# Kernel optimization log

Hardware: AMD Instinct MI355X
Metric: run time of the kernel (lower is better)

The kernel has to match this reference:

```python
import jax, jax.numpy as jnp
import numpy as np

SIGMA = 0.05  # gaussian bandwidth from the source


def _sqdist(a, b):
    # a: [B,N,D], b: [B,M,D] -> [B,N,M] squared euclidean distance
    a2 = jnp.sum(a * a, axis=-1)[:, :, None]
    b2 = jnp.sum(b * b, axis=-1)[:, None, :]
    return a2 + b2 - 2.0 * jnp.einsum('bnd,bmd->bnm', a, b)


def setup_inputs() -> dict:
    key = jax.random.key(0)
    k1, k2, k3, k4 = jax.random.split(key, 4)
    B, N, D = 2, 4096, 32
    points = jax.random.normal(k1, (B, N, 3), dtype=jnp.float32)
    pointfea1 = jax.random.normal(k2, (B, N, D), dtype=jnp.float32)
    pointfea2 = jax.random.normal(k3, (B, N, D), dtype=jnp.float32)
    weights = jax.random.uniform(k4, (B, N), dtype=jnp.float32) / N  # point-cloud mass weights
    return {"points": points, "pointfea1": pointfea1, "pointfea2": pointfea2, "weights": weights}


def reference(points, pointfea1, pointfea2, weights):
    # naive_corres: per-point spatial log-gaussian softmax vs feature log-softmax,
    # weighted squared difference, reduced over both pair axes -> [B]
    x = points / SIGMA
    point_loggauss = jax.nn.log_softmax(-_sqdist(x, x), axis=2)          # [B,N,N]
    fea_logsoftmax = jax.nn.log_softmax(-_sqdist(pointfea1, pointfea2), axis=2)  # [B,N,N]
    diff2 = (jnp.exp(point_loggauss) - jnp.exp(fea_logsoftmax)) ** 2
    l2_loss = jnp.sum(diff2 * weights[:, :, None], axis=2)  # sum over j
    return jnp.sum(l2_loss, axis=1)                          # sum over i -> [B]
```

## Files before the change

kernel.cpp:

```cpp
#include <hip/hip_runtime.h>

#define D    32
#define BLK  256
#define NCH  8
#define SJ   128

#define LOG2E 1.44269504088896340736f

typedef short  short8  __attribute__((ext_vector_type(8)));
typedef float  floatx4 __attribute__((ext_vector_type(4)));

__device__ __forceinline__ short f2bf(float v) {
    union { float f; unsigned u; } x; x.f = v;
    unsigned r = x.u + 0x7fffu + ((x.u >> 16) & 1u);
    return (short)(r >> 16);
}
__device__ __forceinline__ float bf2f(short h) {
    union { float f; unsigned u; } x;
    x.u = ((unsigned)(unsigned short)h) << 16;
    return x.f;
}
__device__ __forceinline__ float fast_exp2(float x) {
#if __has_builtin(__builtin_amdgcn_exp2f)
    return __builtin_amdgcn_exp2f(x);
#else
    return exp2f(x);
#endif
}

__global__ __launch_bounds__(BLK) void precompute_kernel(
    const float* __restrict__ points,
    const float* __restrict__ fea1,
    const float* __restrict__ fea2,
    float4* __restrict__ xp,
    float* __restrict__ f1n,
    float* __restrict__ f2n,
    float* __restrict__ acc,
    float* __restrict__ out,
    int BN, int Bsz)
{
    int r = blockIdx.x * BLK + threadIdx.x;
    if (r < Bsz) out[r] = 0.0f;
    if (r >= BN) return;
#pragma unroll
    for (int s = 0; s < 5; ++s) acc[s * BN + r] = 0.0f;

    const float s20 = 20.0f;
    float x = points[3*r+0] * s20;
    float y = points[3*r+1] * s20;
    float z = points[3*r+2] * s20;
    float4 v; v.x = x; v.y = y; v.z = z;
    v.w = (x*x + y*y + z*z) * LOG2E;
    xp[r] = v;

    const float4* p1 = (const float4*)(fea1 + (size_t)r * D);
    const float4* p2 = (const float4*)(fea2 + (size_t)r * D);
    float n1 = 0.f, n2 = 0.f;
#pragma unroll
    for (int k = 0; k < D/4; ++k) {
        float4 a = p1[k];
        float4 b = p2[k];
        n1 = fmaf(a.x,a.x, fmaf(a.y,a.y, fmaf(a.z,a.z, fmaf(a.w,a.w, n1))));
        n2 = fmaf(b.x,b.x, fmaf(b.y,b.y, fmaf(b.z,b.z, fmaf(b.w,b.w, n2))));
    }
    f1n[r] = n1 * LOG2E;
    f2n[r] = n2 * LOG2E;
}

__global__ __launch_bounds__(BLK) void pair_kernel(
    const float* __restrict__ fea1,
    const float* __restrict__ fea2,
    const float4* __restrict__ xp,
    const float* __restrict__ f1n,
    const float* __restrict__ f2n,
    float* __restrict__ acc,
    int N, int BN)
{
    __shared__ short  sHi[SJ * D];
    __shared__ short  sLo[SJ * D];
    __shared__ float4 sXJ[SJ];
    __shared__ float  sFN[SJ];

    const int tid  = threadIdx.x;
    const int lane = tid & 63;
    const int wv   = tid >> 6;
    const int m    = lane & 15;
    const int q    = lane >> 4;

    const int ibpb  = N / 64;
    const int b     = blockIdx.x / ibpb;
    const int ibase = blockIdx.x * 64 + wv * 16;
    const int JCH   = N / NCH;
    const int jc0   = blockIdx.y * JCH;

    const float* f1p = fea1 + (size_t)(ibase + m) * D + q * 8;
    float4 bv0 = *(const float4*)(f1p);
    float4 bv1 = *(const float4*)(f1p + 4);
    float bf[8] = {bv0.x,bv0.y,bv0.z,bv0.w,bv1.x,bv1.y,bv1.z,bv1.w};
    short8 Bhi, Blo;
#pragma unroll
    for (int k = 0; k < 8; ++k) {
        short h = f2bf(bf[k]);
        Bhi[k] = h;
        Blo[k] = f2bf(bf[k] - bf2f(h));
    }

    const float L2 = 2.0f * LOG2E;
    float4 xi = xp[ibase + m];
    float xix = xi.x * L2, xiy = xi.y * L2, xiz = xi.z * L2, xiw = xi.w;
    float nfi = -f1n[ibase + m];

    float sA = 0.f, s2a = 0.f, sB = 0.f, s2b = 0.f, sab = 0.f;

    const float*  f2b  = fea2 + (size_t)(b * N + jc0) * D;
    const float4* xpb  = xp  + (size_t)b * N + jc0;
    const float*  f2nb = f2n + (size_t)b * N + jc0;

    const int rowl = tid >> 3;
    const int c4   = (tid & 7) * 4;

    for (int s = 0; s < JCH; s += SJ) {
#pragma unroll
        for (int g = 0; g < SJ/32; ++g) {
            int r_ = g * 32 + rowl;
            float4 v = *(const float4*)(f2b + (size_t)(s + r_) * D + c4);
            short4 h, l;
            h.x = f2bf(v.x); l.x = f2bf(v.x - bf2f(h.x));
            h.y = f2bf(v.y); l.y = f2bf(v.y - bf2f(h.y));
            h.z = f2bf(v.z); l.z = f2bf(v.z - bf2f(h.z));
            h.w = f2bf(v.w); l.w = f2bf(v.w - bf2f(h.w));
            *(short4*)&sHi[r_ * D + c4] = h;
            *(short4*)&sLo[r_ * D + c4] = l;
        }
        if (tid < SJ) {
            sXJ[tid] = xpb[s + tid];
            sFN[tid] = f2nb[s + tid];
        }
        __syncthreads();

#pragma unroll 2
        for (int jt = 0; jt < SJ; jt += 16) {
            const short8 Ahi = *(const short8*)&sHi[(jt + m) * D + q * 8];
            const short8 Alo = *(const short8*)&sLo[(jt + m) * D + q * 8];
            floatx4 c = {0.f, 0.f, 0.f, 0.f};
            c = __builtin_amdgcn_mfma_f32_16x16x32_bf16(Ahi, Bhi, c, 0, 0, 0);
            c = __builtin_amdgcn_mfma_f32_16x16x32_bf16(Ahi, Blo, c, 0, 0, 0);
            c = __builtin_amdgcn_mfma_f32_16x16x32_bf16(Alo, Bhi, c, 0, 0, 0);
#pragma unroll
            for (int r = 0; r < 4; ++r) {
                int jl = jt + q * 4 + r;
                float4 xj = sXJ[jl];
                float bL = fmaf(c[r], L2, nfi - sFN[jl]);
                float aL = fmaf(xiz, xj.z,
                            fmaf(xiy, xj.y,
                             fmaf(xix, xj.x, -xiw))) - xj.w;
                float ea = fast_exp2(aL);
                float eb = fast_exp2(bL);
                sA += ea;
                sB += eb;
                s2a = fmaf(ea, ea, s2a);
                s2b = fmaf(eb, eb, s2b);
                sab = fmaf(ea, eb, sab);
            }
        }
        __syncthreads();
    }

    sA  += __shfl_xor(sA, 16);  sA  += __shfl_xor(sA, 32);
    s2a += __shfl_xor(s2a, 16); s2a += __shfl_xor(s2a, 32);
    sB  += __shfl_xor(sB, 16);  sB  += __shfl_xor(sB, 32);
    s2b += __shfl_xor(s2b, 16); s2b += __shfl_xor(s2b, 32);
    sab += __shfl_xor(sab, 16); sab += __shfl_xor(sab, 32);

    if (lane < 16) {
        int row = ibase + lane;
        atomicAdd(&acc[0*BN + row], sA);
        atomicAdd(&acc[1*BN + row], s2a);
        atomicAdd(&acc[2*BN + row], sB);
        atomicAdd(&acc[3*BN + row], s2b);
        atomicAdd(&acc[4*BN + row], sab);
    }
}

__global__ __launch_bounds__(BLK) void finalize_kernel(
    const float* __restrict__ acc,
    const float* __restrict__ weights,
    float* __restrict__ out,
    int N, int BN)
{
    int row = blockIdx.x * BLK + threadIdx.x;
    int b   = (blockIdx.x * BLK) / N;

    float A   = acc[0*BN + row];
    float S2a = acc[1*BN + row];
    float Bt  = acc[2*BN + row];
    float S2b = acc[3*BN + row];
    float Sab = acc[4*BN + row];
    float invA = 1.0f / A;
    float invB = 1.0f / Bt;
    float val  = S2a*invA*invA - 2.0f*Sab*invA*invB + S2b*invB*invB;
    float sum  = weights[row] * val;

    __shared__ float red[BLK/64];
    for (int off = 32; off > 0; off >>= 1)
        sum += __shfl_down(sum, off);
    if ((threadIdx.x & 63) == 0) red[threadIdx.x >> 6] = sum;
    __syncthreads();
    if (threadIdx.x == 0) {
        float s = 0.f;
#pragma unroll
        for (int w = 0; w < BLK/64; ++w) s += red[w];
        atomicAdd(&out[b], s);
    }
}

extern "C" void kernel_launch(void* const* d_in, const int* in_sizes, int n_in,
                              void* d_out, int out_size, void* d_ws, size_t ws_size,
                              hipStream_t stream) {
    const float* points  = (const float*)d_in[0];
    const float* fea1    = (const float*)d_in[1];
    const float* fea2    = (const float*)d_in[2];
    const float* weights = (const float*)d_in[3];
    float* out = (float*)d_out;

    int B  = out_size;
    int BN = in_sizes[3];
    int N  = BN / B;

    float*  acc = (float*)d_ws;
    float4* xp  = (float4*)((char*)d_ws + (size_t)5  * BN * sizeof(float));
    float*  f2n = (float*)((char*)d_ws + (size_t)9  * BN * sizeof(float));
    float*  f1n = (float*)((char*)d_ws + (size_t)10 * BN * sizeof(float));

    precompute_kernel<<<dim3((BN + BLK - 1) / BLK), dim3(BLK), 0, stream>>>(
        points, fea1, fea2, xp, f1n, f2n, acc, out, BN, B);

    dim3 grid(BN / 64, NCH);
    pair_kernel<<<grid, dim3(BLK), 0, stream>>>(
        fea1, fea2, xp, f1n, f2n, acc, N, BN);

    finalize_kernel<<<dim3(BN / BLK), dim3(BLK), 0, stream>>>(acc, weights, out, N, BN);
}
```

Baseline: 90.83 us.

## Precompute bf16 hi/lo split of fea2 in MFMA-ready layout, double j-chunks

The bf16 hi/lo split of fea2 now happens once in the precompute kernel, which writes it to workspace in a layout that matches the MFMA A-operand fragment order. The pair kernel can then fill shared memory with straight 16-byte copies instead of redoing the split for every i-block. The j-axis split count goes from 8 to 16 for more blocks, at the cost of twice as many atomic adds into the accumulators. Per-element sums are packed into float2 vectors so the compiler can emit packed adds and FMAs.

```diff
diff --git a/kernel.cpp b/kernel.cpp
--- a/kernel.cpp
+++ b/kernel.cpp
@@ -2,13 +2,14 @@
 
 #define D    32
 #define BLK  256
-#define NCH  8
+#define NCH  16
 #define SJ   128
 
 #define LOG2E 1.44269504088896340736f
 
 typedef short  short8  __attribute__((ext_vector_type(8)));
 typedef float  floatx4 __attribute__((ext_vector_type(4)));
+typedef float  v2f     __attribute__((ext_vector_type(2)));
 
 __device__ __forceinline__ short f2bf(float v) {
     union { float f; unsigned u; } x; x.f = v;
@@ -35,6 +36,8 @@
     float4* __restrict__ xp,
     float* __restrict__ f1n,
     float* __restrict__ f2n,
+    short* __restrict__ f2hi,
+    short* __restrict__ f2lo,
     float* __restrict__ acc,
     float* __restrict__ out,
     int BN, int Bsz)
@@ -54,30 +57,50 @@
     xp[r] = v;
 
     const float4* p1 = (const float4*)(fea1 + (size_t)r * D);
-    const float4* p2 = (const float4*)(fea2 + (size_t)r * D);
-    float n1 = 0.f, n2 = 0.f;
+    float n1 = 0.f;
 #pragma unroll
     for (int k = 0; k < D/4; ++k) {
         float4 a = p1[k];
-        float4 b = p2[k];
         n1 = fmaf(a.x,a.x, fmaf(a.y,a.y, fmaf(a.z,a.z, fmaf(a.w,a.w, n1))));
-        n2 = fmaf(b.x,b.x, fmaf(b.y,b.y, fmaf(b.z,b.z, fmaf(b.w,b.w, n2))));
     }
     f1n[r] = n1 * LOG2E;
+
+    const int t = r >> 4;
+    const int m = r & 15;
+    const float* p2 = fea2 + (size_t)r * D;
+    float n2 = 0.f;
+#pragma unroll
+    for (int q = 0; q < 4; ++q) {
+        float4 v0 = *(const float4*)(p2 + q*8);
+        float4 v1 = *(const float4*)(p2 + q*8 + 4);
+        float e[8] = {v0.x,v0.y,v0.z,v0.w,v1.x,v1.y,v1.z,v1.w};
+        short8 h, l;
+#pragma unroll
+        for (int k = 0; k < 8; ++k) {
+            n2 = fmaf(e[k], e[k], n2);
+            short hh = f2bf(e[k]);
+            h[k] = hh;
+            l[k] = f2bf(e[k] - bf2f(hh));
+        }
+        size_t off = ((size_t)t * 64 + m + 16*q) * 8;
+        *(short8*)&f2hi[off] = h;
+        *(short8*)&f2lo[off] = l;
+    }
     f2n[r] = n2 * LOG2E;
 }
 
 __global__ __launch_bounds__(BLK) void pair_kernel(
     const float* __restrict__ fea1,
-    const float* __restrict__ fea2,
+    const short* __restrict__ f2hi,
+    const short* __restrict__ f2lo,
     const float4* __restrict__ xp,
     const float* __restrict__ f1n,
     const float* __restrict__ f2n,
     float* __restrict__ acc,
     int N, int BN)
 {
-    __shared__ short  sHi[SJ * D];
-    __shared__ short  sLo[SJ * D];
+    __shared__ __align__(16) short sHi[SJ * D];
+    __shared__ __align__(16) short sLo[SJ * D];
     __shared__ float4 sXJ[SJ];
     __shared__ float  sFN[SJ];
 
@@ -107,31 +130,28 @@
 
     const float L2 = 2.0f * LOG2E;
     float4 xi = xp[ibase + m];
-    float xix = xi.x * L2, xiy = xi.y * L2, xiz = xi.z * L2, xiw = xi.w;
-    float nfi = -f1n[ibase + m];
-
-    float sA = 0.f, s2a = 0.f, sB = 0.f, s2b = 0.f, sab = 0.f;
-
-    const float*  f2b  = fea2 + (size_t)(b * N + jc0) * D;
+    float xix = xi.x * L2, xiy = xi.y * L2, xiz = xi.z * L2;
+    float mxiw = -xi.w;
+    float nfi  = -f1n[ibase + m];
+
+    v2f sAB = {0.f, 0.f};
+    v2f s2  = {0.f, 0.f};
+    float sab = 0.f;
+
+    const short*  gHi  = f2hi + ((size_t)(b * N + jc0) >> 4) * 512;
+    const short*  gLo  = f2lo + ((size_t)(b * N + jc0) >> 4) * 512;
     const float4* xpb  = xp  + (size_t)b * N + jc0;
     const float*  f2nb = f2n + (size_t)b * N + jc0;
 
-    const int rowl = tid >> 3;
-    const int c4   = (tid & 7) * 4;
-
     for (int s = 0; s < JCH; s += SJ) {
-#pragma unroll
-        for (int g = 0; g < SJ/32; ++g) {
-            int r_ = g * 32 + rowl;
-            float4 v = *(const float4*)(f2b + (size_t)(s + r_) * D + c4);
-            short4 h, l;
-            h.x = f2bf(v.x); l.x = f2bf(v.x - bf2f(h.x));
-            h.y = f2bf(v.y); l.y = f2bf(v.y - bf2f(h.y));
-            h.z = f2bf(v.z); l.z = f2bf(v.z - bf2f(h.z));
-            h.w = f2bf(v.w); l.w = f2bf(v.w - bf2f(h.w));
-            *(short4*)&sHi[r_ * D + c4] = h;
-            *(short4*)&sLo[r_ * D + c4] = l;
-        }
+        const uint4* srcH = (const uint4*)(gHi + (size_t)(s >> 4) * 512);
+        const uint4* srcL = (const uint4*)(gLo + (size_t)(s >> 4) * 512);
+        uint4* dstH = (uint4*)sHi;
+        uint4* dstL = (uint4*)sLo;
+        dstH[tid]       = srcH[tid];
+        dstH[tid + 256] = srcH[tid + 256];
+        dstL[tid]       = srcL[tid];
+        dstL[tid + 256] = srcL[tid + 256];
         if (tid < SJ) {
             sXJ[tid] = xpb[s + tid];
             sFN[tid] = f2nb[s + tid];
@@ -139,45 +159,45 @@
         __syncthreads();
 
 #pragma unroll 2
-        for (int jt = 0; jt < SJ; jt += 16) {
-            const short8 Ahi = *(const short8*)&sHi[(jt + m) * D + q * 8];
-            const short8 Alo = *(const short8*)&sLo[(jt + m) * D + q * 8];
+        for (int jt8 = 0; jt8 < SJ/16; ++jt8) {
+            const short8 Ahi = *(const short8*)&sHi[(jt8 * 64 + lane) * 8];
+            const short8 Alo = *(const short8*)&sLo[(jt8 * 64 + lane) * 8];
             floatx4 c = {0.f, 0.f, 0.f, 0.f};
             c = __builtin_amdgcn_mfma_f32_16x16x32_bf16(Ahi, Bhi, c, 0, 0, 0);
             c = __builtin_amdgcn_mfma_f32_16x16x32_bf16(Ahi, Blo, c, 0, 0, 0);
             c = __builtin_amdgcn_mfma_f32_16x16x32_bf16(Alo, Bhi, c, 0, 0, 0);
 #pragma unroll
             for (int r = 0; r < 4; ++r) {
-                int jl = jt + q * 4 + r;
+                int jl = jt8 * 16 + q * 4 + r;
                 float4 xj = sXJ[jl];
                 float bL = fmaf(c[r], L2, nfi - sFN[jl]);
                 float aL = fmaf(xiz, xj.z,
-                            fmaf(xiy, xj.y,
-                             fmaf(xix, xj.x, -xiw))) - xj.w;
+                             fmaf(xiy, xj.y,
+                              fmaf(xix, xj.x, mxiw))) - xj.w;
                 float ea = fast_exp2(aL);
                 float eb = fast_exp2(bL);
-                sA += ea;
-                sB += eb;
-                s2a = fmaf(ea, ea, s2a);
-                s2b = fmaf(eb, eb, s2b);
-                sab = fmaf(ea, eb, sab);
+                v2f e = {ea, eb};
+                sAB += e;
+                s2   = __builtin_elementwise_fma(e, e, s2);
+                sab  = fmaf(ea, eb, sab);
             }
         }
         __syncthreads();
     }
 
-    sA  += __shfl_xor(sA, 16);  sA  += __shfl_xor(sA, 32);
-    s2a += __shfl_xor(s2a, 16); s2a += __shfl_xor(s2a, 32);
-    sB  += __shfl_xor(sB, 16);  sB  += __shfl_xor(sB, 32);
-    s2b += __shfl_xor(s2b, 16); s2b += __shfl_xor(s2b, 32);
+    float vA = sAB.x, vB = sAB.y, v2a = s2.x, v2b = s2.y;
+    vA  += __shfl_xor(vA, 16);  vA  += __shfl_xor(vA, 32);
+    vB  += __shfl_xor(vB, 16);  vB  += __shfl_xor(vB, 32);
+    v2a += __shfl_xor(v2a, 16); v2a += __shfl_xor(v2a, 32);
+    v2b += __shfl_xor(v2b, 16); v2b += __shfl_xor(v2b, 32);
     sab += __shfl_xor(sab, 16); sab += __shfl_xor(sab, 32);
 
     if (lane < 16) {
         int row = ibase + lane;
-        atomicAdd(&acc[0*BN + row], sA);
-        atomicAdd(&acc[1*BN + row], s2a);
-        atomicAdd(&acc[2*BN + row], sB);
-        atomicAdd(&acc[3*BN + row], s2b);
+        atomicAdd(&acc[0*BN + row], vA);
+        atomicAdd(&acc[1*BN + row], v2a);
+        atomicAdd(&acc[2*BN + row], vB);
+        atomicAdd(&acc[3*BN + row], v2b);
         atomicAdd(&acc[4*BN + row], sab);
     }
 }
@@ -227,17 +247,19 @@
     int BN = in_sizes[3];
     int N  = BN / B;
 
-    float*  acc = (float*)d_ws;
-    float4* xp  = (float4*)((char*)d_ws + (size_t)5  * BN * sizeof(float));
-    float*  f2n = (float*)((char*)d_ws + (size_t)9  * BN * sizeof(float));
-    float*  f1n = (float*)((char*)d_ws + (size_t)10 * BN * sizeof(float));
+    float*  acc  = (float*)d_ws;
+    float4* xp   = (float4*)((char*)d_ws + (size_t)5  * BN * 4);
+    float*  f2n  = (float*)((char*)d_ws + (size_t)9  * BN * 4);
+    float*  f1n  = (float*)((char*)d_ws + (size_t)10 * BN * 4);
+    short*  f2hi = (short*)((char*)d_ws + (size_t)11 * BN * 4);
+    short*  f2lo = f2hi + (size_t)BN * D;
 
     precompute_kernel<<<dim3((BN + BLK - 1) / BLK), dim3(BLK), 0, stream>>>(
-        points, fea1, fea2, xp, f1n, f2n, acc, out, BN, B);
+        points, fea1, fea2, xp, f1n, f2n, f2hi, f2lo, acc, out, BN, B);
 
     dim3 grid(BN / 64, NCH);
     pair_kernel<<<grid, dim3(BLK), 0, stream>>>(
-        fea1, fea2, xp, f1n, f2n, acc, N, BN);
+        fea1, f2hi, f2lo, xp, f1n, f2n, acc, N, BN);
 
     finalize_kernel<<<dim3(BN / BLK), dim3(BLK), 0, stream>>>(acc, weights, out, N, BN);
 }
```

Measured after the change: 86.04 us. -5.3%, faster.
